# Kernel tuning notes

Measured on AMD Instinct MI355X. Metric: run time of the kernel, lower is better.

The kernel has to match this reference:

```python
import jax, jax.numpy as jnp
import numpy as np

N_ATOMS = 2048
N_METAL = 512
BOX = (20.0, 20.0, 40.0)   # orthorhombic slab cell (A)
DL = 2.0                    # EwaldPotential dl -> k-grid half-extent per dim
SIGMA = 0.5540037           # 1/1.805132, Gaussian charge width
NMAX = tuple(int(np.ceil(L / DL)) for L in BOX)


def _kgrid():
    # integer reciprocal-lattice grid, k=0 excluded (built once at trace time)
    nx, ny, nz = NMAX
    g = np.stack(np.meshgrid(np.arange(-nx, nx + 1),
                             np.arange(-ny, ny + 1),
                             np.arange(-nz, nz + 1), indexing='ij'), -1).reshape(-1, 3)
    g = g[np.any(g != 0, axis=1)]
    return g.astype(np.float32)

_GRID = _kgrid()  # [K,3]


def ewald_field(r, q, cell):
    """Reciprocal-space Ewald potential phi_i = dE/dq_i for Gaussian-smeared charges.
    r:[N,3] q:[N,C] cell:[3,3] (rows = lattice vectors). Returns [N,C]."""
    V = jnp.abs(jnp.linalg.det(cell))
    recip = 2.0 * jnp.pi * jnp.linalg.inv(cell).T          # rows: reciprocal vectors
    k = jnp.asarray(_GRID, dtype=r.dtype) @ recip          # [K,3]
    k2 = jnp.sum(k * k, axis=-1)                           # [K]
    kfac = jnp.exp(-0.5 * SIGMA * SIGMA * k2) / k2         # exponent=1 kernel
    phase = r @ k.T                                        # [N,K]  (dominant traffic)
    c, s = jnp.cos(phase), jnp.sin(phase)
    cq = kfac[:, None] * (c.T @ q)                         # [K,C]
    sq = kfac[:, None] * (s.T @ q)
    return (4.0 * jnp.pi / V) * (c @ cq + s @ sq)          # [N,C]


def setup_inputs() -> dict:
    key = jax.random.key(0)
    k1, k2 = jax.random.split(key)
    box = jnp.asarray(BOX, dtype=jnp.float32)
    positions = jax.random.uniform(k1, (N_ATOMS, 3), dtype=jnp.float32) * box
    q = jax.random.normal(k2, (N_ATOMS, 1), dtype=jnp.float32) * 0.5
    cell = jnp.diag(box)
    # metal (Z=79) atoms occupy the first N_METAL slots; rest electrolyte (Z=8)
    atomic_numbers = jnp.concatenate([
        jnp.full((N_METAL,), 79, dtype=jnp.int32),
        jnp.full((N_ATOMS - N_METAL,), 8, dtype=jnp.int32)])
    return {"positions": positions, "q": q, "cell": cell,
            "atomic_numbers": atomic_numbers, "n_metal": N_METAL}


def reference(positions, q, cell, atomic_numbers, n_metal):
    nm = int(n_metal)  # static: metal atoms are the first nm rows
    dt = positions.dtype
    # q_all[metal] = 0
    q = q.at[:nm].set(0.0)
    # capacitance matrix S from detached coords (torch uses r.detach(), cell.detach())
    r_m = jax.lax.stop_gradient(positions[:nm])
    cell_d = jax.lax.stop_gradient(cell)
    A = ewald_field(r_m, jnp.eye(nm, dtype=dt), cell_d)     # [nm,nm] A_mat
    A_inv = jnp.linalg.inv(A)
    ones = jnp.ones((nm, 1), dtype=dt)
    Ai1 = A_inv @ ones                                       # [nm,1]
    S = A_inv - (Ai1 @ Ai1.T) / (ones.T @ Ai1)               # charge-neutral projector
    # full-system field; scaling_factor=1, external_field=None -> B_ext = 0
    f = ewald_field(positions, q, cell)                      # [N,1]
    B = -f[:nm]
    q_mw = q.at[:nm].set(S @ B)
    e_corr = jnp.zeros((1,), dtype=dt)   # scaling_factor == 1.0 branch
    e_ext = jnp.zeros((1,), dtype=dt)    # external_field is None
    return q_mw, e_corr, e_ext
```

## Files before the change

kernel.cpp:

```cpp
#include <hip/hip_runtime.h>
#include <math.h>

#define N_ATOMS 2048
#define NM      512
#define KHALF   9040
#define KPAD    9216
#define TWO_PI  6.2831853071795864769f
#define SIGMA   0.5540037f
#define FOUR_PI 12.566370614359172954f

__device__ inline void inv3x3(const float* __restrict__ c, float inv[3][3], float& det) {
    float a00=c[0],a01=c[1],a02=c[2],a10=c[3],a11=c[4],a12=c[5],a20=c[6],a21=c[7],a22=c[8];
    float c00 =  a11*a22 - a12*a21;
    float c01 = -(a10*a22 - a12*a20);
    float c02 =  a10*a21 - a11*a20;
    det = a00*c00 + a01*c01 + a02*c02;
    float id = 1.0f/det;
    inv[0][0] = c00*id;
    inv[0][1] = -(a01*a22 - a02*a21)*id;
    inv[0][2] =  (a01*a12 - a02*a11)*id;
    inv[1][0] = c01*id;
    inv[1][1] =  (a00*a22 - a02*a20)*id;
    inv[1][2] = -(a00*a12 - a02*a10)*id;
    inv[2][0] = c02*id;
    inv[2][1] = -(a00*a21 - a01*a20)*id;
    inv[2][2] =  (a00*a11 - a01*a10)*id;
}

__device__ __forceinline__ void gbar(int* cnt, int* flag, int ph, int G) {
    __syncthreads();
    if (threadIdx.x == 0) {
        __threadfence();
        int prev = __hip_atomic_fetch_add(cnt, 1, __ATOMIC_ACQ_REL, __HIP_MEMORY_SCOPE_AGENT);
        if (prev == G*ph - 1) {
            __hip_atomic_store(flag, ph, __ATOMIC_RELEASE, __HIP_MEMORY_SCOPE_AGENT);
        } else {
            while (__hip_atomic_load(flag, __ATOMIC_RELAXED, __HIP_MEMORY_SCOPE_AGENT) < ph)
                __builtin_amdgcn_s_sleep(4);
        }
        __threadfence();
    }
    __syncthreads();
}

__global__ void prep(const float* __restrict__ pos, const float* __restrict__ qv,
                     const float* __restrict__ cell, float4* __restrict__ kdata,
                     float4* __restrict__ uq, float* __restrict__ out) {
    const int bb = blockIdx.x, tid = threadIdx.x;
    if (bb < 36) {
        int t = bb*256 + tid;
        float gx=0.f, gy=0.f, gz=0.f, wk=0.f;
        if (t < KHALF) {
            int iz = t % 41; int rem = t / 41; int iy = rem % 21; int ix = rem / 21;
            gx = (float)(ix - 10); gy = (float)(iy - 10); gz = (float)(iz - 20);
            float inv[3][3], det;
            inv3x3(cell, inv, det);
            float kx = TWO_PI*(gx*inv[0][0] + gy*inv[0][1] + gz*inv[0][2]);
            float ky = TWO_PI*(gx*inv[1][0] + gy*inv[1][1] + gz*inv[1][2]);
            float kz = TWO_PI*(gx*inv[2][0] + gy*inv[2][1] + gz*inv[2][2]);
            float k2 = kx*kx + ky*ky + kz*kz;
            float kfac = __expf(-0.5f*SIGMA*SIGMA*k2) / k2;
            wk = sqrtf(2.0f*kfac);
        }
        kdata[t] = make_float4(gx, gy, gz, wk);
    } else {
        int i = (bb-36)*256 + tid;
        float inv[3][3], det;
        inv3x3(cell, inv, det);
        float x = pos[3*i], y = pos[3*i+1], z = pos[3*i+2];
        float u = x*inv[0][0] + y*inv[1][0] + z*inv[2][0];
        float v = x*inv[0][1] + y*inv[1][1] + z*inv[2][1];
        float w = x*inv[0][2] + y*inv[1][2] + z*inv[2][2];
        float qi = qv[i];
        uq[i] = make_float4(u, v, w, qi);
        if (i >= NM) out[i] = qi;
        if (i == 0) { out[N_ATOMS] = 0.f; out[N_ATOMS+1] = 0.f; }
    }
}

__global__ void __launch_bounds__(256, 2) syrk_sf(const float4* __restrict__ kdata,
        const float4* __restrict__ uq, float* __restrict__ partial,
        float* __restrict__ Scw, float* __restrict__ Ssw, int SL, int KSL, int nsyrk) {
    __shared__ float smem[16384];
    const int tid = threadIdx.x;
    if ((int)blockIdx.x >= nsyrk) {
        int ch = blockIdx.x - nsyrk;
        int kk = tid & 63, sp = tid >> 6;
        int k = ch*64 + kk;
        float4 kd = kdata[k];
        float sc = 0.f, ss = 0.f;
        int jlo = NM + sp*384, jhi = jlo + 384;
        for (int j = jlo; j < jhi; ++j) {
            float4 at = uq[j];
            float ph = TWO_PI*(kd.x*at.x + kd.y*at.y + kd.z*at.z);
            float s, c; __sincosf(ph, &s, &c);
            sc += at.w * c;
            ss += at.w * s;
        }
        smem[sp*64 + kk] = sc;
        smem[256 + sp*64 + kk] = ss;
        __syncthreads();
        if (sp == 0) {
            float c = smem[kk] + smem[64+kk] + smem[128+kk] + smem[192+kk];
            float s = smem[256+kk] + smem[320+kk] + smem[384+kk] + smem[448+kk];
            float kf2 = kd.w * kd.w;
            Scw[k] = kf2 * c;
            Ssw[k] = kf2 * s;
        }
        return;
    }
    int s = blockIdx.x % SL;
    int t = blockIdx.x / SL;
    int rt = 0;
    while ((rt+1)*(rt+2)/2 <= t) ++rt;
    int ct = t - rt*(rt+1)/2;
    const int row0 = rt << 7, c0 = ct << 7;
    const bool diag = (row0 == c0);
    float* crT = smem; float* srT = smem+4096; float* ccT = smem+8192; float* scT = smem+12288;
    const float* ccR = diag ? crT : ccT;
    const float* scR = diag ? srT : scT;
    const int i0 = (tid & 15) << 3;
    const int j0 = (tid >> 4) << 3;
    float acc[8][8];
    #pragma unroll
    for (int i = 0; i < 8; ++i)
        #pragma unroll
        for (int j = 0; j < 8; ++j) acc[i][j] = 0.f;
    const int k0 = s * KSL;
    const int nch = KSL >> 5;
    for (int ch = 0; ch < nch; ++ch) {
        int kc = k0 + (ch << 5);
        __syncthreads();
        #pragma unroll
        for (int w = 0; w < 16; ++w) {
            int job = tid + (w << 8);
            int kk = job >> 7, a = job & 127;
            float4 kd = kdata[kc + kk];
            float4 at = uq[row0 + a];
            float ph = TWO_PI*(kd.x*at.x + kd.y*at.y + kd.z*at.z);
            float sn, cs;
            __sincosf(ph, &sn, &cs);
            crT[kk*128+a] = kd.w * cs;
            srT[kk*128+a] = kd.w * sn;
        }
        if (!diag) {
            #pragma unroll
            for (int w = 0; w < 16; ++w) {
                int job = tid + (w << 8);
                int kk = job >> 7, a = job & 127;
                float4 kd = kdata[kc + kk];
                float4 at = uq[c0 + a];
                float ph = TWO_PI*(kd.x*at.x + kd.y*at.y + kd.z*at.z);
                float sn, cs;
                __sincosf(ph, &sn, &cs);
                ccT[kk*128+a] = kd.w * cs;
                scT[kk*128+a] = kd.w * sn;
            }
        }
        __syncthreads();
        #pragma unroll 4
        for (int kk = 0; kk < 32; ++kk) {
            float cr[8], sr[8], cc[8], sv[8];
            *(float4*)&cr[0] = *(const float4*)&crT[kk*128+i0];
            *(float4*)&cr[4] = *(const float4*)&crT[kk*128+i0+4];
            *(float4*)&sr[0] = *(const float4*)&srT[kk*128+i0];
            *(float4*)&sr[4] = *(const float4*)&srT[kk*128+i0+4];
            *(float4*)&cc[0] = *(const float4*)&ccR[kk*128+j0];
            *(float4*)&cc[4] = *(const float4*)&ccR[kk*128+j0+4];
            *(float4*)&sv[0] = *(const float4*)&scR[kk*128+j0];
            *(float4*)&sv[4] = *(const float4*)&scR[kk*128+j0+4];
            #pragma unroll
            for (int i = 0; i < 8; ++i)
                #pragma unroll
                for (int j = 0; j < 8; ++j)
                    acc[i][j] += cr[i]*cc[j] + sr[i]*sv[j];
        }
    }
    float* P = partial + ((size_t)blockIdx.x << 14);
    #pragma unroll
    for (int i = 0; i < 8; ++i) {
        *(float4*)&P[(i0+i)*128 + j0]     = make_float4(acc[i][0], acc[i][1], acc[i][2], acc[i][3]);
        *(float4*)&P[(i0+i)*128 + j0 + 4] = make_float4(acc[i][4], acc[i][5], acc[i][6], acc[i][7]);
    }
}

__device__ void diag_fast(float* D, float* T, float* M, int tid, int pd, float* Dinvs) {
    __syncthreads();
    if (tid < 64) {
        float row[64];
        #pragma unroll
        for (int c = 0; c < 64; ++c) row[c] = D[tid*68 + c];
        #pragma unroll
        for (int j = 0; j < 64; ++j) {
            float pj = __shfl(row[j], j);
            float rinv = 1.0f / sqrtf(pj);
            float lj = row[j] * rinv;
            row[j] = lj;
            #pragma unroll
            for (int c = j+1; c < 64; ++c) {
                float lcj = __shfl(lj, c);
                row[c] = fmaf(-lj, lcj, row[c]);
            }
        }
        #pragma unroll
        for (int c = 0; c < 64; ++c) D[tid*68 + c] = row[c];
    }
    __syncthreads();
    for (int idx = tid; idx < 64*68; idx += 256) T[idx] = 0.f;
    __syncthreads();
    if (tid < 64) {
        int s = tid >> 3, c = tid & 7, o = s*8;
        float x[8];
        #pragma unroll
        for (int r = 0; r < 8; ++r) {
            float acc = (r == c) ? 1.0f : 0.0f;
            #pragma unroll
            for (int j = 0; j < 8; ++j)
                if (j < r) acc -= D[(o+r)*68 + o + j] * x[j];
            x[r] = (r >= c) ? acc / D[(o+r)*68 + o + r] : 0.0f;
        }
        #pragma unroll
        for (int r = 0; r < 8; ++r)
            if (r >= c) T[(o+r)*68 + o + c] = x[r];
    }
    __syncthreads();
    #pragma unroll
    for (int lvl = 0; lvl < 3; ++lvl) {
        int h = 8 << lvl, pairs = 4 >> lvl, hh = h*h;
        for (int e = tid; e < pairs*hh; e += 256) {
            int pr = e / hh, rem = e - pr*hh, r2 = rem / h, c2 = rem - (rem/h)*h;
            int o = pr*2*h;
            float acc = 0.f;
            for (int j2 = c2; j2 < h; ++j2)
                acc += D[(o+h+r2)*68 + o + j2] * T[(o+j2)*68 + o + c2];
            M[e] = acc;
        }
        __syncthreads();
        for (int e = tid; e < pairs*hh; e += 256) {
            int pr = e / hh, rem = e - pr*hh, r2 = rem / h, c2 = rem - (rem/h)*h;
            int o = pr*2*h;
            float acc = 0.f;
            for (int j2 = 0; j2 <= r2; ++j2)
                acc += T[(o+h+r2)*68 + o+h + j2] * M[pr*hh + j2*h + c2];
            T[(o+h+r2)*68 + o + c2] = -acc;
        }
        __syncthreads();
    }
    for (int idx = tid; idx < 4096; idx += 256) {
        int r = idx >> 6, c = idx & 63;
        Dinvs[pd*4096 + idx] = (c <= r) ? T[r*68+c] : 0.f;
    }
}

__global__ void __launch_bounds__(256) redfield(const float* __restrict__ partial,
        const float* __restrict__ cell, float* __restrict__ Amat,
        const float4* __restrict__ kdata, const float4* __restrict__ uq,
        const float* __restrict__ Scw, const float* __restrict__ Ssw,
        float* __restrict__ Bvec, int SL) {
    const int b = blockIdx.x, tid = threadIdx.x;
    float inv[3][3], det;
    inv3x3(cell, inv, det);
    const float scal = FOUR_PI / fabsf(det);
    if (b < 512) {
        for (int idx = b*256 + tid; idx < 512*512; idx += 512*256) {
            int i = idx >> 9, j = idx & 511;
            if (i < j) continue;
            int rt2 = i >> 7, ct2 = j >> 7;
            int t2 = rt2*(rt2+1)/2 + ct2;
            const float* p = partial + ((size_t)(t2*SL) << 14) + ((i & 127) << 7) + (j & 127);
            float a0=0.f,a1=0.f,a2=0.f,a3=0.f,a4=0.f,a5=0.f,a6=0.f,a7=0.f;
            int s = 0;
            for (; s + 8 <= SL; s += 8) {
                a0 += p[(size_t)(s+0) << 14];
                a1 += p[(size_t)(s+1) << 14];
                a2 += p[(size_t)(s+2) << 14];
                a3 += p[(size_t)(s+3) << 14];
                a4 += p[(size_t)(s+4) << 14];
                a5 += p[(size_t)(s+5) << 14];
                a6 += p[(size_t)(s+6) << 14];
                a7 += p[(size_t)(s+7) << 14];
            }
            for (; s < SL; ++s) a0 += p[(size_t)s << 14];
            float sum = ((a0+a1)+(a2+a3)) + ((a4+a5)+(a6+a7));
            float v = scal * sum;
            Amat[(size_t)i*512 + j] = v;
            Amat[(size_t)j*512 + i] = v;
        }
    } else {
        int ch = b - 512;
        int atom = ch*4 + (tid >> 6);
        int lane = tid & 63;
        float4 at = uq[atom];
        float acc = 0.f;
        for (int k = lane; k < KPAD; k += 64) {
            float4 kd = kdata[k];
            float ph = TWO_PI*(kd.x*at.x + kd.y*at.y + kd.z*at.z);
            float s, c; __sincosf(ph, &s, &c);
            acc += c*Scw[k] + s*Ssw[k];
        }
        #pragma unroll
        for (int off = 32; off; off >>= 1) acc += __shfl_down(acc, off);
        if (lane == 0) Bvec[atom] = -scal * acc;
    }
}

__global__ void __launch_bounds__(256) tail_persist(float* __restrict__ Amat,
        float* __restrict__ Lmat, float* __restrict__ LmatT, float* __restrict__ Dinvs,
        const float* __restrict__ Bvec, float* __restrict__ out,
        int* cnt, int* flag) {
    __shared__ float smem[15360];
    const int b = blockIdx.x, tid = threadIdx.x;
    const int G = 28;

    if (b == 0) {
        float* D = smem; float* T = smem + 4352; float* M = smem + 8704;
        for (int idx = tid; idx < 4096; idx += 256) {
            int r = idx >> 6, c = idx & 63;
            D[r*68+c] = Amat[(size_t)r*512 + c];
        }
        diag_fast(D, T, M, tid, 0, Dinvs);
    }
    gbar(cnt, flag, 1, G);

    for (int p = 0; p <= 6; ++p) {
        const int T7 = 7 - p, ntile = T7*(T7+1)/2;
        if (b < ntile) {
            const int tt = b;
            int rt = 0; while ((rt+1)*(rt+2)/2 <= tt) ++rt;
            const int ct = tt - rt*(rt+1)/2;
            const int R = p + 1 + rt, C = p + 1 + ct;
            float* ArT = smem;
            float* DvT = smem + 4352;
            float* LrT = smem + 8704;
            float* LcT = smem + 13056;
            float pref[16];
            if (R != C) {
                #pragma unroll
                for (int w = 0; w < 16; ++w) {
                    int idx = tid + (w << 8);
                    pref[w] = Amat[(size_t)(C*64 + (idx >> 6))*512 + p*64 + (idx & 63)];
                }
            }
            __syncthreads();
            for (int idx = tid; idx < 4096; idx += 256) {
                int j = idx >> 6, d = idx & 63;
                DvT[d*68 + j] = Dinvs[p*4096 + j*64 + d];
            }
            for (int idx = tid; idx < 4096; idx += 256) {
                int i = idx >> 6, k = idx & 63;
                ArT[k*68 + i] = Amat[(size_t)(R*64 + i)*512 + p*64 + k];
            }
            __syncthreads();
            const int i0 = (tid & 15)*4, j0 = (tid >> 4)*4;
            float lr[4][4];
            #pragma unroll
            for (int ii = 0; ii < 4; ++ii)
                #pragma unroll
                for (int jj = 0; jj < 4; ++jj) lr[ii][jj] = 0.f;
            for (int k = 0; k < 64; ++k) {
                float4 av = *(float4*)&ArT[k*68 + i0];
                float4 dv = *(float4*)&DvT[k*68 + j0];
                lr[0][0] += av.x*dv.x; lr[0][1] += av.x*dv.y; lr[0][2] += av.x*dv.z; lr[0][3] += av.x*dv.w;
                lr[1][0] += av.y*dv.x; lr[1][1] += av.y*dv.y; lr[1][2] += av.y*dv.z; lr[1][3] += av.y*dv.w;
                lr[2][0] += av.z*dv.x; lr[2][1] += av.z*dv.y; lr[2][2] += av.z*dv.z; lr[2][3] += av.z*dv.w;
                lr[3][0] += av.w*dv.x; lr[3][1] += av.w*dv.y; lr[3][2] += av.w*dv.z; lr[3][3] += av.w*dv.w;
            }
            #pragma unroll
            for (int ii = 0; ii < 4; ++ii)
                #pragma unroll
                for (int jj = 0; jj < 4; ++jj)
                    LrT[(j0+jj)*68 + i0+ii] = lr[ii][jj];
            __syncthreads();
            if (C == p + 1) {
                for (int idx = tid; idx < 4096; idx += 256) {
                    int i2 = idx >> 6, c2 = idx & 63;
                    Lmat[(size_t)(R*64+i2)*512 + p*64 + c2] = LrT[c2*68 + i2];
                }
                for (int idx = tid; idx < 4096; idx += 256) {
                    int c2 = idx >> 6, i2 = idx & 63;
                    LmatT[(size_t)(p*64+c2)*512 + R*64 + i2] = LrT[c2*68 + i2];
                }
            }
            if (R == C) {
                float up[4][4];
                #pragma unroll
                for (int ii = 0; ii < 4; ++ii)
                    #pragma unroll
                    for (int jj = 0; jj < 4; ++jj) up[ii][jj] = 0.f;
                for (int k = 0; k < 64; ++k) {
                    float4 av = *(float4*)&LrT[k*68 + i0];
                    float4 bv = *(float4*)&LrT[k*68 + j0];
                    up[0][0] += av.x*bv.x; up[0][1] += av.x*bv.y; up[0][2] += av.x*bv.z; up[0][3] += av.x*bv.w;
                    up[1][0] += av.y*bv.x; up[1][1] += av.y*bv.y; up[1][2] += av.y*bv.z; up[1][3] += av.y*bv.w;
                    up[2][0] += av.z*bv.x; up[2][1] += av.z*bv.y; up[2][2] += av.z*bv.z; up[2][3] += av.z*bv.w;
                    up[3][0] += av.w*bv.x; up[3][1] += av.w*bv.y; up[3][2] += av.w*bv.z; up[3][3] += av.w*bv.w;
                }
                float vals[4][4];
                #pragma unroll
                for (int ii = 0; ii < 4; ++ii)
                    #pragma unroll
                    for (int jj = 0; jj < 4; ++jj) {
                        size_t gix = (size_t)(R*64+i0+ii)*512 + C*64 + j0 + jj;
                        float v = Amat[gix] - up[ii][jj];
                        Amat[gix] = v;
                        vals[ii][jj] = v;
                    }
                if (tt == 0) {
                    float* D = smem; float* T = smem + 4352; float* M = smem + 8704;
                    __syncthreads();
                    #pragma unroll
                    for (int ii = 0; ii < 4; ++ii)
                        #pragma unroll
                        for (int jj = 0; jj < 4; ++jj)
                            D[(i0+ii)*68 + j0+jj] = vals[ii][jj];
                    diag_fast(D, T, M, tid, p+1, Dinvs);
                }
            } else {
                for (int w = 0; w < 16; ++w) {
                    int idx = tid + (w << 8);
                    ArT[(idx & 63)*68 + (idx >> 6)] = pref[w];
                }
                __syncthreads();
                const int c0l = (tid & 15)*4, jr0 = (tid >> 4)*2;
                #pragma unroll
                for (int hh = 0; hh < 2; ++hh) {
                    float lc[4][2];
                    #pragma unroll
                    for (int cc = 0; cc < 4; ++cc) { lc[cc][0] = 0.f; lc[cc][1] = 0.f; }
                    for (int d = 0; d < 64; ++d) {
                        float4 dv = *(float4*)&DvT[d*68 + c0l];
                        float2 av = *(float2*)&ArT[d*68 + hh*32 + jr0];
                        lc[0][0] += dv.x*av.x; lc[0][1] += dv.x*av.y;
                        lc[1][0] += dv.y*av.x; lc[1][1] += dv.y*av.y;
                        lc[2][0] += dv.z*av.x; lc[2][1] += dv.z*av.y;
                        lc[3][0] += dv.w*av.x; lc[3][1] += dv.w*av.y;
                    }
                    __syncthreads();
                    #pragma unroll
                    for (int cc = 0; cc < 4; ++cc) {
                        LcT[(c0l+cc)*36 + jr0]     = lc[cc][0];
                        LcT[(c0l+cc)*36 + jr0 + 1] = lc[cc][1];
                    }
                    __syncthreads();
                    float up[4][2];
                    #pragma unroll
                    for (int ii = 0; ii < 4; ++ii) { up[ii][0] = 0.f; up[ii][1] = 0.f; }
                    for (int c2 = 0; c2 < 64; ++c2) {
                        float4 lv = *(float4*)&LrT[c2*68 + i0];
                        float2 cv = *(float2*)&LcT[c2*36 + jr0];
                        up[0][0] += lv.x*cv.x; up[0][1] += lv.x*cv.y;
                        up[1][0] += lv.y*cv.x; up[1][1] += lv.y*cv.y;
                        up[2][0] += lv.z*cv.x; up[2][1] += lv.z*cv.y;
                        up[3][0] += lv.w*cv.x; up[3][1] += lv.w*cv.y;
                    }
                    #pragma unroll
                    for (int ii = 0; ii < 4; ++ii)
                        #pragma unroll
                        for (int jr = 0; jr < 2; ++jr) {
                            size_t gix = (size_t)(R*64+i0+ii)*512 + C*64 + hh*32 + jr0 + jr;
                            Amat[gix] -= up[ii][jr];
                        }
                }
            }
        }
        gbar(cnt, flag, p + 2, G);
    }

    if (b == 0) {
        float* rb  = smem;
        float* ro  = smem + 512;
        float* xb  = smem + 1024;
        float* xo  = smem + 1536;
        float* bvs = smem + 2048;
        float* red = smem + 2560;
        __syncthreads();
        for (int i = tid; i < 512; i += 256) {
            float bv = Bvec[i];
            bvs[i] = bv; rb[i] = bv; ro[i] = 1.0f;
        }
        __syncthreads();
        for (int k = 0; k < 8; ++k) {
            if (tid < 64) {
                const float* Dk = Dinvs + k*4096 + tid*64;
                float s1 = 0.f, s2 = 0.f;
                for (int c4 = 0; c4 < 16; ++c4) {
                    float4 w = *(const float4*)&Dk[c4*4];
                    int cb = 64*k + c4*4;
                    s1 += w.x*rb[cb] + w.y*rb[cb+1] + w.z*rb[cb+2] + w.w*rb[cb+3];
                    s2 += w.x*ro[cb] + w.y*ro[cb+1] + w.z*ro[cb+2] + w.w*ro[cb+3];
                }
                rb[64*k+tid] = s1; ro[64*k+tid] = s2;
            }
            __syncthreads();
            for (int mm = 64*(k+1) + tid; mm < 512; mm += 256) {
                const float* Lr = Lmat + (size_t)mm*512 + 64*k;
                float s1 = 0.f, s2 = 0.f;
                for (int c4 = 0; c4 < 16; ++c4) {
                    float4 l = *(const float4*)&Lr[c4*4];
                    int cb = 64*k + c4*4;
                    s1 += l.x*rb[cb] + l.y*rb[cb+1] + l.z*rb[cb+2] + l.w*rb[cb+3];
                    s2 += l.x*ro[cb] + l.y*ro[cb+1] + l.z*ro[cb+2] + l.w*ro[cb+3];
                }
                rb[mm] -= s1; ro[mm] -= s2;
            }
            __syncthreads();
        }
        for (int k = 7; k >= 0; --k) {
            if (tid < 64) {
                const float* D0 = Dinvs + k*4096;
                float s1 = 0.f, s2 = 0.f;
                for (int c = 0; c < 64; ++c) {
                    float w = D0[c*64 + tid];
                    s1 += w*rb[64*k+c]; s2 += w*ro[64*k+c];
                }
                xb[64*k+tid] = s1; xo[64*k+tid] = s2;
            }
            __syncthreads();
            for (int mm = tid; mm < 64*k; mm += 256) {
                const float* Ur = LmatT + (size_t)mm*512 + 64*k;
                float s1 = 0.f, s2 = 0.f;
                for (int c4 = 0; c4 < 16; ++c4) {
                    float4 u = *(const float4*)&Ur[c4*4];
                    int cb = 64*k + c4*4;
                    s1 += u.x*xb[cb] + u.y*xb[cb+1] + u.z*xb[cb+2] + u.w*xb[cb+3];
                    s2 += u.x*xo[cb] + u.y*xo[cb+1] + u.z*xo[cb+2] + u.w*xo[cb+3];
                }
                rb[mm] -= s1; ro[mm] -= s2;
            }
            __syncthreads();
        }
        float pn = 0.f, pd = 0.f;
        for (int i = tid; i < 512; i += 256) { pn += xo[i]*bvs[i]; pd += xo[i]; }
        #pragma unroll
        for (int off = 32; off; off >>= 1) { pn += __shfl_down(pn, off); pd += __shfl_down(pd, off); }
        if ((tid & 63) == 0) { red[tid >> 6] = pn; red[4 + (tid >> 6)] = pd; }
        __syncthreads();
        if (tid == 0) {
            float sn = red[0]+red[1]+red[2]+red[3];
            float sd = red[4]+red[5]+red[6]+red[7];
            red[8] = sn / sd;
        }
        __syncthreads();
        float ratio = red[8];
        for (int i = tid; i < 512; i += 256) out[i] = xb[i] - xo[i]*ratio;
    }
}

extern "C" void kernel_launch(void* const* d_in, const int* in_sizes, int n_in,
                              void* d_out, int out_size, void* d_ws, size_t ws_size,
                              hipStream_t stream) {
    (void)in_sizes; (void)n_in; (void)out_size;
    const float* pos  = (const float*)d_in[0];
    const float* qv   = (const float*)d_in[1];
    const float* cell = (const float*)d_in[2];
    float* out = (float*)d_out;
    char* ws = (char*)d_ws;
    size_t off = 0;
    auto alloc = [&](size_t bytes) -> void* {
        void* p = (void*)(ws + off);
        off = (off + bytes + 255) & ~(size_t)255;
        return p;
    };
    float4* kdata = (float4*)alloc((size_t)KPAD*16);
    float4* uq    = (float4*)alloc((size_t)N_ATOMS*16);
    float*  Scw   = (float*)alloc((size_t)KPAD*4);
    float*  Ssw   = (float*)alloc((size_t)KPAD*4);
    float*  Bvec  = (float*)alloc(512*4);
    float*  Amat  = (float*)alloc((size_t)512*512*4);
    float*  Lmat  = (float*)alloc((size_t)512*512*4);
    float*  LmatT = (float*)alloc((size_t)512*512*4);
    float*  Dinvs = (float*)alloc((size_t)8*4096*4);
    int* bar = (int*)alloc(256);
    static const int slopts[10] = {96, 72, 48, 36, 24, 16, 12, 8, 4, 1};
    int SL = 1;
    for (int ci = 0; ci < 10; ++ci) {
        size_t need = (size_t)10 * slopts[ci] * 16384 * 4;
        if (off + need <= ws_size) { SL = slopts[ci]; break; }
    }
    float* partial = (float*)alloc((size_t)10*SL*16384*4);
    const int KSL = KPAD / SL;
    const int nsyrk = 10*SL;

    hipMemsetAsync(bar, 0, 8, stream);
    prep<<<dim3(44), dim3(256), 0, stream>>>(pos, qv, cell, kdata, uq, out);
    syrk_sf<<<dim3(nsyrk + 144), dim3(256), 0, stream>>>(kdata, uq, partial,
                                                         Scw, Ssw, SL, KSL, nsyrk);
    redfield<<<dim3(640), dim3(256), 0, stream>>>(partial, cell, Amat, kdata, uq,
                                                  Scw, Ssw, Bvec, SL);
    tail_persist<<<dim3(28), dim3(256), 0, stream>>>(Amat, Lmat, LmatT, Dinvs,
                                                     Bvec, out, bar, bar + 1);
}
```

Before: 648.7 us.

## Replace multi-block persistent Cholesky with single-block 512-thread factor and solve

Replaces the 28-block persistent tail kernel, which used a software grid barrier between panel steps, with a single 512-thread block. That block performs the blocked Cholesky factorization, the diagonal-block inversions and the triangular solves sequentially, which removes the atomic spin barriers and the barrier-counter memset. L is now stored in place in Amat rather than in a separate Lmat. In exchange, all trailing-update tile work is serialized on one CU instead of spread across up to 28 blocks.

```diff
diff --git a/kernel.cpp b/kernel.cpp
--- a/kernel.cpp
+++ b/kernel.cpp
@@ -25,22 +25,6 @@
     inv[2][0] = c02*id;
     inv[2][1] = -(a00*a21 - a01*a20)*id;
     inv[2][2] =  (a00*a11 - a01*a10)*id;
-}
-
-__device__ __forceinline__ void gbar(int* cnt, int* flag, int ph, int G) {
-    __syncthreads();
-    if (threadIdx.x == 0) {
-        __threadfence();
-        int prev = __hip_atomic_fetch_add(cnt, 1, __ATOMIC_ACQ_REL, __HIP_MEMORY_SCOPE_AGENT);
-        if (prev == G*ph - 1) {
-            __hip_atomic_store(flag, ph, __ATOMIC_RELEASE, __HIP_MEMORY_SCOPE_AGENT);
-        } else {
-            while (__hip_atomic_load(flag, __ATOMIC_RELAXED, __HIP_MEMORY_SCOPE_AGENT) < ph)
-                __builtin_amdgcn_s_sleep(4);
-        }
-        __threadfence();
-    }
-    __syncthreads();
 }
 
 __global__ void prep(const float* __restrict__ pos, const float* __restrict__ qv,
@@ -181,74 +165,6 @@
     for (int i = 0; i < 8; ++i) {
         *(float4*)&P[(i0+i)*128 + j0]     = make_float4(acc[i][0], acc[i][1], acc[i][2], acc[i][3]);
         *(float4*)&P[(i0+i)*128 + j0 + 4] = make_float4(acc[i][4], acc[i][5], acc[i][6], acc[i][7]);
-    }
-}
-
-__device__ void diag_fast(float* D, float* T, float* M, int tid, int pd, float* Dinvs) {
-    __syncthreads();
-    if (tid < 64) {
-        float row[64];
-        #pragma unroll
-        for (int c = 0; c < 64; ++c) row[c] = D[tid*68 + c];
-        #pragma unroll
-        for (int j = 0; j < 64; ++j) {
-            float pj = __shfl(row[j], j);
-            float rinv = 1.0f / sqrtf(pj);
-            float lj = row[j] * rinv;
-            row[j] = lj;
-            #pragma unroll
-            for (int c = j+1; c < 64; ++c) {
-                float lcj = __shfl(lj, c);
-                row[c] = fmaf(-lj, lcj, row[c]);
-            }
-        }
-        #pragma unroll
-        for (int c = 0; c < 64; ++c) D[tid*68 + c] = row[c];
-    }
-    __syncthreads();
-    for (int idx = tid; idx < 64*68; idx += 256) T[idx] = 0.f;
-    __syncthreads();
-    if (tid < 64) {
-        int s = tid >> 3, c = tid & 7, o = s*8;
-        float x[8];
-        #pragma unroll
-        for (int r = 0; r < 8; ++r) {
-            float acc = (r == c) ? 1.0f : 0.0f;
-            #pragma unroll
-            for (int j = 0; j < 8; ++j)
-                if (j < r) acc -= D[(o+r)*68 + o + j] * x[j];
-            x[r] = (r >= c) ? acc / D[(o+r)*68 + o + r] : 0.0f;
-        }
-        #pragma unroll
-        for (int r = 0; r < 8; ++r)
-            if (r >= c) T[(o+r)*68 + o + c] = x[r];
-    }
-    __syncthreads();
-    #pragma unroll
-    for (int lvl = 0; lvl < 3; ++lvl) {
-        int h = 8 << lvl, pairs = 4 >> lvl, hh = h*h;
-        for (int e = tid; e < pairs*hh; e += 256) {
-            int pr = e / hh, rem = e - pr*hh, r2 = rem / h, c2 = rem - (rem/h)*h;
-            int o = pr*2*h;
-            float acc = 0.f;
-            for (int j2 = c2; j2 < h; ++j2)
-                acc += D[(o+h+r2)*68 + o + j2] * T[(o+j2)*68 + o + c2];
-            M[e] = acc;
-        }
-        __syncthreads();
-        for (int e = tid; e < pairs*hh; e += 256) {
-            int pr = e / hh, rem = e - pr*hh, r2 = rem / h, c2 = rem - (rem/h)*h;
-            int o = pr*2*h;
-            float acc = 0.f;
-            for (int j2 = 0; j2 <= r2; ++j2)
-                acc += T[(o+h+r2)*68 + o+h + j2] * M[pr*hh + j2*h + c2];
-            T[(o+h+r2)*68 + o + c2] = -acc;
-        }
-        __syncthreads();
-    }
-    for (int idx = tid; idx < 4096; idx += 256) {
-        int r = idx >> 6, c = idx & 63;
-        Dinvs[pd*4096 + idx] = (c <= r) ? T[r*68+c] : 0.f;
     }
 }
 
@@ -304,177 +220,177 @@
     }
 }
 
-__global__ void __launch_bounds__(256) tail_persist(float* __restrict__ Amat,
-        float* __restrict__ Lmat, float* __restrict__ LmatT, float* __restrict__ Dinvs,
-        const float* __restrict__ Bvec, float* __restrict__ out,
-        int* cnt, int* flag) {
-    __shared__ float smem[15360];
-    const int b = blockIdx.x, tid = threadIdx.x;
-    const int G = 28;
-
-    if (b == 0) {
-        float* D = smem; float* T = smem + 4352; float* M = smem + 8704;
-        for (int idx = tid; idx < 4096; idx += 256) {
-            int r = idx >> 6, c = idx & 63;
-            D[r*68+c] = Amat[(size_t)r*512 + c];
-        }
-        diag_fast(D, T, M, tid, 0, Dinvs);
-    }
-    gbar(cnt, flag, 1, G);
-
-    for (int p = 0; p <= 6; ++p) {
-        const int T7 = 7 - p, ntile = T7*(T7+1)/2;
-        if (b < ntile) {
-            const int tt = b;
-            int rt = 0; while ((rt+1)*(rt+2)/2 <= tt) ++rt;
-            const int ct = tt - rt*(rt+1)/2;
-            const int R = p + 1 + rt, C = p + 1 + ct;
-            float* ArT = smem;
-            float* DvT = smem + 4352;
-            float* LrT = smem + 8704;
-            float* LcT = smem + 13056;
-            float pref[16];
-            if (R != C) {
-                #pragma unroll
-                for (int w = 0; w < 16; ++w) {
-                    int idx = tid + (w << 8);
-                    pref[w] = Amat[(size_t)(C*64 + (idx >> 6))*512 + p*64 + (idx & 63)];
-                }
-            }
-            __syncthreads();
-            for (int idx = tid; idx < 4096; idx += 256) {
-                int j = idx >> 6, d = idx & 63;
-                DvT[d*68 + j] = Dinvs[p*4096 + j*64 + d];
-            }
-            for (int idx = tid; idx < 4096; idx += 256) {
+__device__ void pivot_factor(float* smem, float* TT, int tid, int p,
+                             float* Amat, float* Dinvs) {
+    float* D = smem + 4352;
+    float* T = smem + 8704;
+    float* M = smem + 13056;
+    for (int idx = tid; idx < 4096; idx += 512) {
+        int r = idx >> 6, c = idx & 63;
+        D[r*68+c] = Amat[(size_t)(p*64+r)*512 + p*64 + c];
+    }
+    __syncthreads();
+    if (tid < 64) {
+        float row[64];
+        #pragma unroll
+        for (int c = 0; c < 64; ++c) row[c] = D[tid*68 + c];
+        #pragma unroll
+        for (int j = 0; j < 64; ++j) {
+            float pj = __shfl(row[j], j);
+            float rinv = 1.0f / sqrtf(pj);
+            float lj = row[j] * rinv;
+            row[j] = lj;
+            #pragma unroll
+            for (int c = j+1; c < 64; ++c) {
+                float lcj = __shfl(lj, c);
+                row[c] = fmaf(-lj, lcj, row[c]);
+            }
+        }
+        #pragma unroll
+        for (int c = 0; c < 64; ++c) D[tid*68 + c] = row[c];
+    }
+    __syncthreads();
+    for (int idx = tid; idx < 64*68; idx += 512) T[idx] = 0.f;
+    __syncthreads();
+    if (tid < 64) {
+        int s = tid >> 3, c = tid & 7, o = s*8;
+        float x[8];
+        #pragma unroll
+        for (int r = 0; r < 8; ++r) {
+            float acc = (r == c) ? 1.0f : 0.0f;
+            #pragma unroll
+            for (int j = 0; j < 8; ++j)
+                if (j < r) acc -= D[(o+r)*68 + o + j] * x[j];
+            x[r] = (r >= c) ? acc / D[(o+r)*68 + o + r] : 0.0f;
+        }
+        #pragma unroll
+        for (int r = 0; r < 8; ++r)
+            if (r >= c) T[(o+r)*68 + o + c] = x[r];
+    }
+    __syncthreads();
+    #pragma unroll
+    for (int lvl = 0; lvl < 3; ++lvl) {
+        int h = 8 << lvl, pairs = 4 >> lvl, hh = h*h;
+        for (int e = tid; e < pairs*hh; e += 512) {
+            int pr = e / hh, rem = e - pr*hh, r2 = rem / h, c2 = rem - (rem/h)*h;
+            int o = pr*2*h;
+            float acc = 0.f;
+            for (int j2 = c2; j2 < h; ++j2)
+                acc += D[(o+h+r2)*68 + o + j2] * T[(o+j2)*68 + o + c2];
+            M[e] = acc;
+        }
+        __syncthreads();
+        for (int e = tid; e < pairs*hh; e += 512) {
+            int pr = e / hh, rem = e - pr*hh, r2 = rem / h, c2 = rem - (rem/h)*h;
+            int o = pr*2*h;
+            float acc = 0.f;
+            for (int j2 = 0; j2 <= r2; ++j2)
+                acc += T[(o+h+r2)*68 + o+h + j2] * M[pr*hh + j2*h + c2];
+            T[(o+h+r2)*68 + o + c2] = -acc;
+        }
+        __syncthreads();
+    }
+    for (int idx = tid; idx < 4096; idx += 512) {
+        int r = idx >> 6, c = idx & 63;
+        float v = (c <= r) ? T[r*68+c] : 0.f;
+        TT[c*64 + r] = v;
+        Dinvs[p*4096 + idx] = v;
+    }
+    __syncthreads();
+}
+
+__global__ void __launch_bounds__(512) chol_solve(float* __restrict__ Amat,
+        float* __restrict__ LmatT, float* __restrict__ Dinvs,
+        const float* __restrict__ Bvec, float* __restrict__ out) {
+    __shared__ float smem[14080];
+    float* TT = smem;
+    const int tid = threadIdx.x;
+    const int i0 = (tid & 15)*4, q0 = (tid >> 4)*2;
+
+    for (int p = 0; p < 8; ++p) {
+        pivot_factor(smem, TT, tid, p, Amat, Dinvs);
+        float* ArS = smem + 4352;
+        float* LrS = smem + 8704;
+        float* LcS = smem + 4352;
+        for (int R = p+1; R < 8; ++R) {
+            __syncthreads();
+            for (int idx = tid; idx < 4096; idx += 512) {
                 int i = idx >> 6, k = idx & 63;
-                ArT[k*68 + i] = Amat[(size_t)(R*64 + i)*512 + p*64 + k];
-            }
-            __syncthreads();
-            const int i0 = (tid & 15)*4, j0 = (tid >> 4)*4;
-            float lr[4][4];
-            #pragma unroll
-            for (int ii = 0; ii < 4; ++ii)
-                #pragma unroll
-                for (int jj = 0; jj < 4; ++jj) lr[ii][jj] = 0.f;
+                ArS[k*68 + i] = Amat[(size_t)(R*64+i)*512 + p*64 + k];
+            }
+            __syncthreads();
+            float lr[4][2];
+            #pragma unroll
+            for (int ii = 0; ii < 4; ++ii) { lr[ii][0] = 0.f; lr[ii][1] = 0.f; }
             for (int k = 0; k < 64; ++k) {
-                float4 av = *(float4*)&ArT[k*68 + i0];
-                float4 dv = *(float4*)&DvT[k*68 + j0];
-                lr[0][0] += av.x*dv.x; lr[0][1] += av.x*dv.y; lr[0][2] += av.x*dv.z; lr[0][3] += av.x*dv.w;
-                lr[1][0] += av.y*dv.x; lr[1][1] += av.y*dv.y; lr[1][2] += av.y*dv.z; lr[1][3] += av.y*dv.w;
-                lr[2][0] += av.z*dv.x; lr[2][1] += av.z*dv.y; lr[2][2] += av.z*dv.z; lr[2][3] += av.z*dv.w;
-                lr[3][0] += av.w*dv.x; lr[3][1] += av.w*dv.y; lr[3][2] += av.w*dv.z; lr[3][3] += av.w*dv.w;
-            }
-            #pragma unroll
-            for (int ii = 0; ii < 4; ++ii)
-                #pragma unroll
-                for (int jj = 0; jj < 4; ++jj)
-                    LrT[(j0+jj)*68 + i0+ii] = lr[ii][jj];
-            __syncthreads();
-            if (C == p + 1) {
-                for (int idx = tid; idx < 4096; idx += 256) {
-                    int i2 = idx >> 6, c2 = idx & 63;
-                    Lmat[(size_t)(R*64+i2)*512 + p*64 + c2] = LrT[c2*68 + i2];
-                }
-                for (int idx = tid; idx < 4096; idx += 256) {
-                    int c2 = idx >> 6, i2 = idx & 63;
-                    LmatT[(size_t)(p*64+c2)*512 + R*64 + i2] = LrT[c2*68 + i2];
-                }
-            }
-            if (R == C) {
-                float up[4][4];
-                #pragma unroll
-                for (int ii = 0; ii < 4; ++ii)
-                    #pragma unroll
-                    for (int jj = 0; jj < 4; ++jj) up[ii][jj] = 0.f;
-                for (int k = 0; k < 64; ++k) {
-                    float4 av = *(float4*)&LrT[k*68 + i0];
-                    float4 bv = *(float4*)&LrT[k*68 + j0];
-                    up[0][0] += av.x*bv.x; up[0][1] += av.x*bv.y; up[0][2] += av.x*bv.z; up[0][3] += av.x*bv.w;
-                    up[1][0] += av.y*bv.x; up[1][1] += av.y*bv.y; up[1][2] += av.y*bv.z; up[1][3] += av.y*bv.w;
-                    up[2][0] += av.z*bv.x; up[2][1] += av.z*bv.y; up[2][2] += av.z*bv.z; up[2][3] += av.z*bv.w;
-                    up[3][0] += av.w*bv.x; up[3][1] += av.w*bv.y; up[3][2] += av.w*bv.z; up[3][3] += av.w*bv.w;
-                }
-                float vals[4][4];
-                #pragma unroll
-                for (int ii = 0; ii < 4; ++ii)
-                    #pragma unroll
-                    for (int jj = 0; jj < 4; ++jj) {
-                        size_t gix = (size_t)(R*64+i0+ii)*512 + C*64 + j0 + jj;
-                        float v = Amat[gix] - up[ii][jj];
-                        Amat[gix] = v;
-                        vals[ii][jj] = v;
-                    }
-                if (tt == 0) {
-                    float* D = smem; float* T = smem + 4352; float* M = smem + 8704;
+                float4 av = *(float4*)&ArS[k*68 + i0];
+                float2 dv = *(float2*)&TT[k*64 + q0];
+                lr[0][0] += av.x*dv.x; lr[0][1] += av.x*dv.y;
+                lr[1][0] += av.y*dv.x; lr[1][1] += av.y*dv.y;
+                lr[2][0] += av.z*dv.x; lr[2][1] += av.z*dv.y;
+                lr[3][0] += av.w*dv.x; lr[3][1] += av.w*dv.y;
+            }
+            __syncthreads();
+            #pragma unroll
+            for (int ii = 0; ii < 4; ++ii) {
+                LrS[(q0+0)*68 + i0+ii] = lr[ii][0];
+                LrS[(q0+1)*68 + i0+ii] = lr[ii][1];
+            }
+            __syncthreads();
+            for (int idx = tid; idx < 4096; idx += 512) {
+                int i2 = idx >> 6, c2 = idx & 63;
+                Amat[(size_t)(R*64+i2)*512 + p*64 + c2] = LrS[c2*68 + i2];
+            }
+            for (int idx = tid; idx < 4096; idx += 512) {
+                int c2 = idx >> 6, i2 = idx & 63;
+                LmatT[(size_t)(p*64+c2)*512 + R*64 + i2] = LrS[c2*68 + i2];
+            }
+            for (int C = p+1; C <= R; ++C) {
+                const float* Lc;
+                if (C == R) {
+                    Lc = LrS;
+                } else {
                     __syncthreads();
-                    #pragma unroll
-                    for (int ii = 0; ii < 4; ++ii)
-                        #pragma unroll
-                        for (int jj = 0; jj < 4; ++jj)
-                            D[(i0+ii)*68 + j0+jj] = vals[ii][jj];
-                    diag_fast(D, T, M, tid, p+1, Dinvs);
-                }
-            } else {
-                for (int w = 0; w < 16; ++w) {
-                    int idx = tid + (w << 8);
-                    ArT[(idx & 63)*68 + (idx >> 6)] = pref[w];
-                }
-                __syncthreads();
-                const int c0l = (tid & 15)*4, jr0 = (tid >> 4)*2;
-                #pragma unroll
-                for (int hh = 0; hh < 2; ++hh) {
-                    float lc[4][2];
-                    #pragma unroll
-                    for (int cc = 0; cc < 4; ++cc) { lc[cc][0] = 0.f; lc[cc][1] = 0.f; }
-                    for (int d = 0; d < 64; ++d) {
-                        float4 dv = *(float4*)&DvT[d*68 + c0l];
-                        float2 av = *(float2*)&ArT[d*68 + hh*32 + jr0];
-                        lc[0][0] += dv.x*av.x; lc[0][1] += dv.x*av.y;
-                        lc[1][0] += dv.y*av.x; lc[1][1] += dv.y*av.y;
-                        lc[2][0] += dv.z*av.x; lc[2][1] += dv.z*av.y;
-                        lc[3][0] += dv.w*av.x; lc[3][1] += dv.w*av.y;
+                    for (int idx = tid; idx < 4096; idx += 512) {
+                        int j2 = idx >> 6, c2 = idx & 63;
+                        LcS[c2*68 + j2] = Amat[(size_t)(C*64+j2)*512 + p*64 + c2];
                     }
                     __syncthreads();
-                    #pragma unroll
-                    for (int cc = 0; cc < 4; ++cc) {
-                        LcT[(c0l+cc)*36 + jr0]     = lc[cc][0];
-                        LcT[(c0l+cc)*36 + jr0 + 1] = lc[cc][1];
-                    }
-                    __syncthreads();
-                    float up[4][2];
-                    #pragma unroll
-                    for (int ii = 0; ii < 4; ++ii) { up[ii][0] = 0.f; up[ii][1] = 0.f; }
-                    for (int c2 = 0; c2 < 64; ++c2) {
-                        float4 lv = *(float4*)&LrT[c2*68 + i0];
-                        float2 cv = *(float2*)&LcT[c2*36 + jr0];
-                        up[0][0] += lv.x*cv.x; up[0][1] += lv.x*cv.y;
-                        up[1][0] += lv.y*cv.x; up[1][1] += lv.y*cv.y;
-                        up[2][0] += lv.z*cv.x; up[2][1] += lv.z*cv.y;
-                        up[3][0] += lv.w*cv.x; up[3][1] += lv.w*cv.y;
-                    }
-                    #pragma unroll
-                    for (int ii = 0; ii < 4; ++ii)
-                        #pragma unroll
-                        for (int jr = 0; jr < 2; ++jr) {
-                            size_t gix = (size_t)(R*64+i0+ii)*512 + C*64 + hh*32 + jr0 + jr;
-                            Amat[gix] -= up[ii][jr];
-                        }
-                }
-            }
-        }
-        gbar(cnt, flag, p + 2, G);
-    }
-
-    if (b == 0) {
-        float* rb  = smem;
-        float* ro  = smem + 512;
-        float* xb  = smem + 1024;
-        float* xo  = smem + 1536;
-        float* bvs = smem + 2048;
-        float* red = smem + 2560;
-        __syncthreads();
-        for (int i = tid; i < 512; i += 256) {
+                    Lc = LcS;
+                }
+                float up[4][2];
+                #pragma unroll
+                for (int ii = 0; ii < 4; ++ii) { up[ii][0] = 0.f; up[ii][1] = 0.f; }
+                for (int c2 = 0; c2 < 64; ++c2) {
+                    float4 lv = *(float4*)&LrS[c2*68 + i0];
+                    float2 cv = *(float2*)&Lc[c2*68 + q0];
+                    up[0][0] += lv.x*cv.x; up[0][1] += lv.x*cv.y;
+                    up[1][0] += lv.y*cv.x; up[1][1] += lv.y*cv.y;
+                    up[2][0] += lv.z*cv.x; up[2][1] += lv.z*cv.y;
+                    up[3][0] += lv.w*cv.x; up[3][1] += lv.w*cv.y;
+                }
+                #pragma unroll
+                for (int ii = 0; ii < 4; ++ii) {
+                    size_t g0 = (size_t)(R*64+i0+ii)*512 + C*64 + q0;
+                    Amat[g0]     -= up[ii][0];
+                    Amat[g0 + 1] -= up[ii][1];
+                }
+            }
+            __threadfence();
+            __syncthreads();
+        }
+    }
+
+    {
+        float* rb  = smem + 4352;
+        float* ro  = smem + 4864;
+        float* xb  = smem + 5376;
+        float* xo  = smem + 5888;
+        float* bvs = smem + 6400;
+        float* red = smem + 6912;
+        __threadfence();
+        __syncthreads();
+        for (int i = tid; i < 512; i += 512) {
             float bv = Bvec[i];
             bvs[i] = bv; rb[i] = bv; ro[i] = 1.0f;
         }
@@ -492,8 +408,8 @@
                 rb[64*k+tid] = s1; ro[64*k+tid] = s2;
             }
             __syncthreads();
-            for (int mm = 64*(k+1) + tid; mm < 512; mm += 256) {
-                const float* Lr = Lmat + (size_t)mm*512 + 64*k;
+            for (int mm = 64*(k+1) + tid; mm < 512; mm += 512) {
+                const float* Lr = Amat + (size_t)mm*512 + 64*k;
                 float s1 = 0.f, s2 = 0.f;
                 for (int c4 = 0; c4 < 16; ++c4) {
                     float4 l = *(const float4*)&Lr[c4*4];
@@ -516,7 +432,7 @@
                 xb[64*k+tid] = s1; xo[64*k+tid] = s2;
             }
             __syncthreads();
-            for (int mm = tid; mm < 64*k; mm += 256) {
+            for (int mm = tid; mm < 64*k; mm += 512) {
                 const float* Ur = LmatT + (size_t)mm*512 + 64*k;
                 float s1 = 0.f, s2 = 0.f;
                 for (int c4 = 0; c4 < 16; ++c4) {
@@ -530,19 +446,20 @@
             __syncthreads();
         }
         float pn = 0.f, pd = 0.f;
-        for (int i = tid; i < 512; i += 256) { pn += xo[i]*bvs[i]; pd += xo[i]; }
+        for (int i = tid; i < 512; i += 512) { pn += xo[i]*bvs[i]; pd += xo[i]; }
         #pragma unroll
         for (int off = 32; off; off >>= 1) { pn += __shfl_down(pn, off); pd += __shfl_down(pd, off); }
-        if ((tid & 63) == 0) { red[tid >> 6] = pn; red[4 + (tid >> 6)] = pd; }
+        if ((tid & 63) == 0) { red[tid >> 6] = pn; red[8 + (tid >> 6)] = pd; }
         __syncthreads();
         if (tid == 0) {
-            float sn = red[0]+red[1]+red[2]+red[3];
-            float sd = red[4]+red[5]+red[6]+red[7];
-            red[8] = sn / sd;
-        }
-        __syncthreads();
-        float ratio = red[8];
-        for (int i = tid; i < 512; i += 256) out[i] = xb[i] - xo[i]*ratio;
+            float sn = 0.f, sd = 0.f;
+            #pragma unroll
+            for (int i = 0; i < 8; ++i) { sn += red[i]; sd += red[8+i]; }
+            red[16] = sn / sd;
+        }
+        __syncthreads();
+        float ratio = red[16];
+        for (int i = tid; i < 512; i += 512) out[i] = xb[i] - xo[i]*ratio;
     }
 }
 
@@ -567,10 +484,8 @@
     float*  Ssw   = (float*)alloc((size_t)KPAD*4);
     float*  Bvec  = (float*)alloc(512*4);
     float*  Amat  = (float*)alloc((size_t)512*512*4);
-    float*  Lmat  = (float*)alloc((size_t)512*512*4);
     float*  LmatT = (float*)alloc((size_t)512*512*4);
     float*  Dinvs = (float*)alloc((size_t)8*4096*4);
-    int* bar = (int*)alloc(256);
     static const int slopts[10] = {96, 72, 48, 36, 24, 16, 12, 8, 4, 1};
     int SL = 1;
     for (int ci = 0; ci < 10; ++ci) {
@@ -581,12 +496,10 @@
     const int KSL = KPAD / SL;
     const int nsyrk = 10*SL;
 
-    hipMemsetAsync(bar, 0, 8, stream);
     prep<<<dim3(44), dim3(256), 0, stream>>>(pos, qv, cell, kdata, uq, out);
     syrk_sf<<<dim3(nsyrk + 144), dim3(256), 0, stream>>>(kdata, uq, partial,
                                                          Scw, Ssw, SL, KSL, nsyrk);
     redfield<<<dim3(640), dim3(256), 0, stream>>>(partial, cell, Amat, kdata, uq,
                                                   Scw, Ssw, Bvec, SL);
-    tail_persist<<<dim3(28), dim3(256), 0, stream>>>(Amat, Lmat, LmatT, Dinvs,
-                                                     Bvec, out, bar, bar + 1);
-}
+    chol_solve<<<dim3(1), dim3(512), 0, stream>>>(Amat, LmatT, Dinvs, Bvec, out);
+}
```

After: 978.6 us. +50.9%, slower.
